# Performance work log

Hardware: AMD Instinct MI355X
Metric: run time of the kernel (lower is better)

Reference implementation:

```python
import jax, jax.numpy as jnp
import numpy as np

B, T, I, H, F = 1024, 15, 256, 512, 8  # batch, seq(=BatchNorm1d(15)), input, hidden, out_features
G = 4 * H  # gate width, PyTorch gate order i,f,g,o


def setup_inputs() -> dict:
    key = jax.random.key(0)
    ks = jax.random.split(key, 10)
    s = lambda k, shape, sc=0.05: (jax.random.normal(k, shape, jnp.float32) * sc)
    return {
        "X": jax.random.normal(ks[0], (B, T, I), jnp.float32),
        # per-head stacked LSTM params (layer 0 and layer 1); bias = b_ih + b_hh combined
        "Wih0": s(ks[1], (F, G, I)), "Whh0": s(ks[2], (F, G, H)), "b0": s(ks[3], (F, G)),
        "Wih1": s(ks[4], (F, G, H)), "Whh1": s(ks[5], (F, G, H)), "b1": s(ks[6], (F, G)),
        # shared affine head: Linear(H,H) -> BatchNorm1d(15) -> ReLU -> Linear(H,1)
        "A1": s(ks[7], (H, H)), "c1": jnp.zeros((H,), jnp.float32),
        "gamma": jnp.ones((T,), jnp.float32), "beta": jnp.zeros((T,), jnp.float32),
        "A2": s(ks[8], (1, H)), "c2": jnp.zeros((1,), jnp.float32),
    }


def _lstm_layer(x, Wih, Whh, b):
    # x: [B,T,Din] -> [B,T,H]; PyTorch LSTM cell, gates ordered i,f,g,o
    xg = jnp.einsum('bti,gi->btg', x, Wih) + b  # precompute input projections [B,T,4H]
    Hh = Whh.shape[1]

    def step(carry, xg_t):
        h, c = carry
        g = xg_t + h @ Whh.T
        i_, f_, g_, o_ = jnp.split(g, 4, axis=-1)
        c = jax.nn.sigmoid(f_) * c + jax.nn.sigmoid(i_) * jnp.tanh(g_)
        h = jax.nn.sigmoid(o_) * jnp.tanh(c)
        return (h, c), h

    h0 = jnp.zeros((x.shape[0], Hh), x.dtype)
    _, hs = jax.lax.scan(step, (h0, h0), jnp.swapaxes(xg, 0, 1))
    return jnp.swapaxes(hs, 0, 1)  # [B,T,H]


def reference(X, Wih0, Whh0, b0, Wih1, Whh1, b1, A1, c1, gamma, beta, A2, c2):
    # F independent 2-layer LSTM stacks, vmapped over the head dim
    def per_head(wih0, whh0, bb0, wih1, whh1, bb1):
        y = _lstm_layer(X, wih0, whh0, bb0)
        return _lstm_layer(y, wih1, whh1, bb1)

    Y = jax.vmap(per_head)(Wih0, Whh0, b0, Wih1, Whh1, b1)  # [F,B,T,H]

    # shared affine head applied per head output (BN stats per head, training mode)
    h1 = jnp.einsum('fbth,oh->fbto', Y, A1) + c1            # [F,B,T,H]
    mean = h1.mean(axis=(1, 3), keepdims=True)              # per (head, channel=T)
    var = h1.var(axis=(1, 3), keepdims=True)                # biased var (torch BN train)
    hn = (h1 - mean) * jax.lax.rsqrt(var + 1e-5)
    hn = hn * gamma[None, None, :, None] + beta[None, None, :, None]
    out = jnp.einsum('fbth,oh->fbto', jax.nn.relu(hn), A2) + c2  # [F,B,T,1]
    return jnp.squeeze(out, -1).transpose(1, 2, 0)          # [B,T,F]
```

## Files before the change

### kernel.cpp

```cpp
#include <hip/hip_runtime.h>
#include <hip/hip_bf16.h>
#include <math.h>

#define Bb 1024
#define Tt 15
#define Ii 256
#define Hh 512
#define Ff 8
#define Gg 2048

typedef __attribute__((ext_vector_type(8))) short short8v;
typedef __attribute__((ext_vector_type(4))) float f32x4;

typedef const __attribute__((address_space(1))) void* gas_ptr;
typedef __attribute__((address_space(3))) void* las_ptr;

__device__ __forceinline__ float sigmoidf_(float x) {
    return __builtin_amdgcn_rcpf(1.0f + __expf(-x));
}
__device__ __forceinline__ float tanhf_(float x) {
    x = fminf(fmaxf(x, -15.0f), 15.0f);
    const float e = __expf(2.0f * x);
    return (e - 1.0f) * __builtin_amdgcn_rcpf(e + 1.0f);
}
__device__ __forceinline__ float bf2f(unsigned short u) {
    return __uint_as_float(((unsigned int)u) << 16);
}
__device__ __forceinline__ unsigned short f2bf(float f) {
    unsigned int u = __float_as_uint(f);
    u += 0x7fffu + ((u >> 16) & 1u);
    return (unsigned short)(u >> 16);
}

__global__ __launch_bounds__(256) void cvt_kernel(const float* __restrict__ in,
                                                  unsigned short* __restrict__ out, int n8) {
    const int i = blockIdx.x * 256 + threadIdx.x;
    if (i < n8) {
        const float4 v0 = ((const float4*)in)[i * 2];
        const float4 v1 = ((const float4*)in)[i * 2 + 1];
        union { unsigned short u[8]; short8v v; } ob;
        ob.u[0] = f2bf(v0.x); ob.u[1] = f2bf(v0.y); ob.u[2] = f2bf(v0.z); ob.u[3] = f2bf(v0.w);
        ob.u[4] = f2bf(v1.x); ob.u[5] = f2bf(v1.y); ob.u[6] = f2bf(v1.z); ob.u[7] = f2bf(v1.w);
        *(short8v*)&out[(size_t)i * 8] = ob.v;
    }
}

__global__ __launch_bounds__(256) void cvt_wperm_kernel(const float* __restrict__ in,
                                                        unsigned short* __restrict__ out,
                                                        int Kc, int nchunks) {
    const int i = blockIdx.x * 256 + threadIdx.x;
    if (i < nchunks) {
        const int k8 = i % Kc;
        const int r  = (i / Kc) & 127;
        const int hb = (i / (Kc * 128)) & 15;
        const int f  = i / (Kc * 128 * 16);
        const int gate = (r >> 4) & 3;
        const int hl = (r & 15) + ((r >> 6) << 4);
        const size_t src = ((size_t)f * Gg + gate * Hh + hb * 32 + hl) * (size_t)(Kc * 8) + k8 * 8;
        const float4 v0 = *(const float4*)(in + src);
        const float4 v1 = *(const float4*)(in + src + 4);
        union { unsigned short u[8]; short8v v; } ob;
        ob.u[0] = f2bf(v0.x); ob.u[1] = f2bf(v0.y); ob.u[2] = f2bf(v0.z); ob.u[3] = f2bf(v0.w);
        ob.u[4] = f2bf(v1.x); ob.u[5] = f2bf(v1.y); ob.u[6] = f2bf(v1.z); ob.u[7] = f2bf(v1.w);
        *(short8v*)&out[(size_t)i * 8] = ob.v;
    }
}

template<int MODE>
__device__ __forceinline__ void step_body(
    bool first, int f, int h0, int b0, int t, int hb, int bb,
    const short* ax, long axs, const short* ah, long ahs,
    const short* __restrict__ wxp, const short* __restrict__ whp,
    const float* __restrict__ bias, unsigned short* __restrict__ cbuf,
    unsigned short* __restrict__ ydst,
    float* __restrict__ part, char* smem)
{
    constexpr int KX = (MODE == 0) ? Ii : Hh;
    constexpr int NX = KX / 64;
    const int NT = (MODE == 2) ? NX : (first ? NX : NX + Hh / 64);

    const int tid = threadIdx.x;
    const int wave = tid >> 6, lane = tid & 63;
    const int wm = (wave >> 1) * 64, wn = (wave & 1) * 64;

    short* sStage = (short*)smem;
    float* pr = (float*)(smem + 65536);

    f32x4 acc[4][4];
#pragma unroll
    for (int i = 0; i < 4; ++i)
#pragma unroll
        for (int j = 0; j < 4; ++j) acc[i][j] = (f32x4){0.f, 0.f, 0.f, 0.f};

    const int srow8 = lane >> 3;
    const int csrc  = (lane & 7) ^ srow8;
    const int frow  = lane & 15, fks = lane >> 4;

    auto stage = [&](int it, int buf) {
        const short* abase; long as; const short* wbase; int K; int kb;
        if (it < NX) { abase = ax; as = axs; wbase = wxp; K = KX; kb = it * 64; }
        else         { abase = ah; as = ahs; wbase = whp; K = Hh; kb = (it - NX) * 64; }
        short* dA = sStage + buf * 16384;
        short* dB = dA + 8192;
#pragma unroll
        for (int i = 0; i < 4; ++i) {
            const int inst = wave * 4 + i;
            const int row = inst * 8 + srow8;
            const short* srcA = abase + (size_t)row * as + kb + csrc * 8;
            __builtin_amdgcn_global_load_lds((gas_ptr)(const void*)srcA,
                (las_ptr)(void*)(dA + inst * 512), 16, 0, 0);
            const short* srcB = wbase + (size_t)row * K + kb + csrc * 8;
            __builtin_amdgcn_global_load_lds((gas_ptr)(const void*)srcB,
                (las_ptr)(void*)(dB + inst * 512), 16, 0, 0);
        }
    };

    auto compute = [&](int buf) {
        const short* bA = sStage + buf * 16384;
        const short* bB = bA + 8192;
        __builtin_amdgcn_s_setprio(1);
#pragma unroll
        for (int ks = 0; ks < 2; ++ks) {
            short8v av[4], bv[4];
#pragma unroll
            for (int i = 0; i < 4; ++i) {
                const int r = wm + i * 16 + frow;
                av[i] = *(const short8v*)&bA[r * 64 + (((fks + ks * 4) ^ (r & 7)) * 8)];
            }
#pragma unroll
            for (int j = 0; j < 4; ++j) {
                const int r = wn + j * 16 + frow;
                bv[j] = *(const short8v*)&bB[r * 64 + (((fks + ks * 4) ^ (r & 7)) * 8)];
            }
#pragma unroll
            for (int i = 0; i < 4; ++i)
#pragma unroll
                for (int j = 0; j < 4; ++j)
                    acc[i][j] = __builtin_amdgcn_mfma_f32_16x16x32_bf16(av[i], bv[j], acc[i][j], 0, 0, 0);
        }
        __builtin_amdgcn_s_setprio(0);
    };

    const int hoff = ((wn >> 6) << 4) + (lane & 15);
    float bi[4] = {0.f, 0.f, 0.f, 0.f};
    if constexpr (MODE != 2) {
#pragma unroll
        for (int g = 0; g < 4; ++g) bi[g] = bias[(size_t)f * Gg + g * Hh + h0 + hoff];
    } else {
#pragma unroll
        for (int j = 0; j < 4; ++j) bi[j] = bias[h0 + wn + j * 16 + (lane & 15)];
    }
    asm volatile("" : "+v"(bi[0]), "+v"(bi[1]), "+v"(bi[2]), "+v"(bi[3]));

    stage(0, 0);
    for (int it = 0; it < NT; ++it) {
        if (it + 1 < NT) {
            stage(it + 1, (it + 1) & 1);
            asm volatile("s_waitcnt vmcnt(8)" ::: "memory");
        } else {
            asm volatile("s_waitcnt vmcnt(0)" ::: "memory");
        }
        __builtin_amdgcn_s_barrier();
        __builtin_amdgcn_sched_barrier(0);
        compute(it & 1);
        __builtin_amdgcn_sched_barrier(0);
        __builtin_amdgcn_s_barrier();
    }

    if constexpr (MODE != 2) {
#pragma unroll
        for (int i = 0; i < 4; ++i)
#pragma unroll
            for (int r = 0; r < 4; ++r) {
                const int b = b0 + wm + i * 16 + ((lane >> 4) << 2) + r;
                const float gi = acc[i][0][r] + bi[0];
                const float gf = acc[i][1][r] + bi[1];
                const float gg = acc[i][2][r] + bi[2];
                const float go = acc[i][3][r] + bi[3];
                const size_t cidx = ((size_t)f * Bb + b) * Hh + h0 + hoff;
                const float cold = first ? 0.f : bf2f(cbuf[cidx]);
                const float cn = sigmoidf_(gf) * cold + sigmoidf_(gi) * tanhf_(gg);
                const float hv = sigmoidf_(go) * tanhf_(cn);
                cbuf[cidx] = f2bf(cn);
                const unsigned short hb2 = f2bf(hv);
                if (MODE == 0)
                    ydst[(((size_t)f * Bb + b) * Tt + t) * Hh + h0 + hoff] = hb2;
                else
                    ydst[cidx] = hb2;
            }
    } else {
        float ssum = 0.f, ssq = 0.f;
#pragma unroll
        for (int i = 0; i < 4; ++i)
#pragma unroll
            for (int r = 0; r < 4; ++r) {
                const int b = b0 + wm + i * 16 + ((lane >> 4) << 2) + r;
                unsigned short* dst = ydst + (((size_t)f * Bb + b) * Tt + t) * Hh;
#pragma unroll
                for (int j = 0; j < 4; ++j) {
                    const int o = h0 + wn + j * 16 + (lane & 15);
                    const unsigned short hb2 = f2bf(acc[i][j][r] + bi[j]);
                    const float hv = bf2f(hb2);
                    ssum += hv; ssq += hv * hv;
                    dst[o] = hb2;
                }
            }
#pragma unroll
        for (int off2 = 32; off2 > 0; off2 >>= 1) {
            ssum += __shfl_down(ssum, off2);
            ssq  += __shfl_down(ssq,  off2);
        }
        if (lane == 0) { pr[wave * 2] = ssum; pr[wave * 2 + 1] = ssq; }
        __syncthreads();
        if (tid == 0) {
            float S = 0.f, Q = 0.f;
#pragma unroll
            for (int w = 0; w < 4; ++w) { S += pr[w * 2]; Q += pr[w * 2 + 1]; }
            const size_t pi = (((size_t)f * Tt + t) * 4 + hb) * 8 + bb;
            part[pi * 2] = S; part[pi * 2 + 1] = Q;
        }
    }
}

__global__ __launch_bounds__(256) void step_merged(
    const short* __restrict__ Xbf, short* __restrict__ ybuf,
    short* __restrict__ h1A, short* __restrict__ h1B,
    const short* __restrict__ W0x, const short* __restrict__ W0h,
    const short* __restrict__ W1x, const short* __restrict__ W1h,
    const short* __restrict__ A1bf,
    const float* __restrict__ b0p, const float* __restrict__ b1p,
    const float* __restrict__ c1v,
    unsigned short* __restrict__ c0buf, unsigned short* __restrict__ c1buf,
    float* __restrict__ part, int d)
{
    __shared__ __align__(16) char smem[65600];
    const int f = blockIdx.x;
    const int zz = blockIdx.z;

    if (zz < 8) {
        const int t = d;
        if (t >= Tt) return;
        const int hb = blockIdx.y, h0 = hb * 32, b0 = zz * 128;
        const bool first = (t == 0);
        const short* ax = Xbf + ((size_t)b0 * Tt + t) * Ii;
        const short* ah = first ? nullptr
                                : ybuf + (((size_t)f * Bb + b0) * Tt + (t - 1)) * Hh;
        step_body<0>(first, f, h0, b0, t, hb, zz,
                     ax, (long)Tt * Ii, ah, (long)Tt * Hh,
                     W0x + ((size_t)f * 16 + hb) * 128 * Ii,
                     W0h + ((size_t)f * 16 + hb) * 128 * Hh,
                     b0p, c0buf, (unsigned short*)ybuf, part, smem);
    } else if (zz < 16) {
        const int t = d - 1;
        if (t < 0 || t >= Tt) return;
        const int bb = zz - 8;
        const int hb = blockIdx.y, h0 = hb * 32, b0 = bb * 128;
        const bool first = (t == 0);
        short* hn = (t & 1) ? h1A : h1B;
        const short* hp = (t & 1) ? h1B : h1A;
        const short* ax = ybuf + (((size_t)f * Bb + b0) * Tt + t) * Hh;
        const short* ah = first ? nullptr : hp + ((size_t)f * Bb + b0) * Hh;
        step_body<1>(first, f, h0, b0, t, hb, bb,
                     ax, (long)Tt * Hh, ah, (long)Hh,
                     W1x + ((size_t)f * 16 + hb) * 128 * Hh,
                     W1h + ((size_t)f * 16 + hb) * 128 * Hh,
                     b1p, c1buf, (unsigned short*)hn, part, smem);
    } else {
        const int t = d - 2;
        if (t < 0) return;
        const int hb = blockIdx.y & 3, h0 = hb * 128;
        const int bb = (zz - 16) * 4 + (blockIdx.y >> 2), b0 = bb * 128;
        const short* hn = (t & 1) ? h1A : h1B;
        const short* ax = hn + ((size_t)f * Bb + b0) * Hh;
        step_body<2>(false, f, h0, b0, t, hb, bb,
                     ax, (long)Hh, nullptr, 0L,
                     A1bf + (size_t)h0 * Hh, nullptr,
                     c1v, nullptr, (unsigned short*)ybuf, part, smem);
    }
}

__global__ void stats_combine_kernel(const float* __restrict__ part, float* __restrict__ stats)
{
    const int i = threadIdx.x;
    if (i < Ff * Tt) {
        float s = 0.f, q = 0.f;
        for (int j = 0; j < 32; ++j) { s += part[(i * 32 + j) * 2]; q += part[(i * 32 + j) * 2 + 1]; }
        const float n = (float)((size_t)Bb * Hh);
        const float mean = s / n;
        const float var  = q / n - mean * mean;
        stats[i * 2]     = mean;
        stats[i * 2 + 1] = rsqrtf(var + 1e-5f);
    }
}

__global__ __launch_bounds__(256) void out_kernel(
    const unsigned short* __restrict__ htmp, const float* __restrict__ stats,
    const float* __restrict__ gamma, const float* __restrict__ beta,
    const float* __restrict__ A2, const float* __restrict__ c2,
    float* __restrict__ out)
{
    const int wave = threadIdx.x >> 6;
    const int lane = threadIdx.x & 63;
    const size_t row = (size_t)blockIdx.x * 4 + wave;
    const int t = (int)(row % Tt);
    const size_t fb = row / Tt;
    const int b = (int)(fb % Bb);
    const int f = (int)(fb / Bb);

    const float mean = stats[(f * Tt + t) * 2];
    const float inv  = stats[(f * Tt + t) * 2 + 1];
    const float ga = gamma[t], be = beta[t];
    const unsigned short* hrow = htmp + row * Hh;

    union { float4 f4; unsigned short u[8]; } hv;
    hv.f4 = *(const float4*)(hrow + lane * 8);
    const float4 a0 = *(const float4*)(A2 + lane * 8);
    const float4 a1 = *(const float4*)(A2 + lane * 8 + 4);
    const float a2v[8] = {a0.x, a0.y, a0.z, a0.w, a1.x, a1.y, a1.z, a1.w};

    float acc = 0.f;
#pragma unroll
    for (int j = 0; j < 8; ++j) {
        const float x = (bf2f(hv.u[j]) - mean) * inv * ga + be;
        acc += fmaxf(x, 0.f) * a2v[j];
    }
#pragma unroll
    for (int off = 32; off > 0; off >>= 1) acc += __shfl_down(acc, off);
    if (lane == 0) out[(size_t)b * Tt * Ff + (size_t)t * Ff + f] = acc + c2[0];
}

extern "C" void kernel_launch(void* const* d_in, const int* in_sizes, int n_in,
                              void* d_out, int out_size, void* d_ws, size_t ws_size,
                              hipStream_t stream) {
    const float* X     = (const float*)d_in[0];
    const float* Wih0  = (const float*)d_in[1];
    const float* Whh0  = (const float*)d_in[2];
    const float* b0p   = (const float*)d_in[3];
    const float* Wih1  = (const float*)d_in[4];
    const float* Whh1  = (const float*)d_in[5];
    const float* b1p   = (const float*)d_in[6];
    const float* A1    = (const float*)d_in[7];
    const float* c1v   = (const float*)d_in[8];
    const float* gamma = (const float*)d_in[9];
    const float* beta  = (const float*)d_in[10];
    const float* A2    = (const float*)d_in[11];
    const float* c2    = (const float*)d_in[12];
    float* out = (float*)d_out;

    char* ws = (char*)d_ws;
    size_t off = 0;
    short* Xbf    = (short*)(ws + off); off += (size_t)Bb * Tt * Ii * 2;
    short* Wih0bf = (short*)(ws + off); off += (size_t)Ff * Gg * Ii * 2;
    short* Whh0bf = (short*)(ws + off); off += (size_t)Ff * Gg * Hh * 2;
    short* Wih1bf = (short*)(ws + off); off += (size_t)Ff * Gg * Hh * 2;
    short* Whh1bf = (short*)(ws + off); off += (size_t)Ff * Gg * Hh * 2;
    short* A1bf   = (short*)(ws + off); off += (size_t)Hh * Hh * 2;
    short* ybuf   = (short*)(ws + off); off += (size_t)Ff * Bb * Tt * Hh * 2;
    short* h1A    = (short*)(ws + off); off += (size_t)Ff * Bb * Hh * 2;
    short* h1B    = (short*)(ws + off); off += (size_t)Ff * Bb * Hh * 2;
    unsigned short* c0buf = (unsigned short*)(ws + off); off += (size_t)Ff * Bb * Hh * 2;
    unsigned short* c1buf = (unsigned short*)(ws + off); off += (size_t)Ff * Bb * Hh * 2;
    float* part   = (float*)(ws + off); off += (size_t)Ff * Tt * 32 * 2 * 4;
    float* stats  = (float*)(ws + off); off += (size_t)Ff * Tt * 2 * 4;

    const dim3 blk(256);
    cvt_kernel<<<dim3((Bb * Tt * Ii / 8 + 255) / 256), blk, 0, stream>>>(X, (unsigned short*)Xbf, Bb * Tt * Ii / 8);
    cvt_wperm_kernel<<<dim3((Ff * Gg * Ii / 8 + 255) / 256), blk, 0, stream>>>(
        Wih0, (unsigned short*)Wih0bf, Ii / 8, Ff * Gg * Ii / 8);
    cvt_wperm_kernel<<<dim3((Ff * Gg * Hh / 8 + 255) / 256), blk, 0, stream>>>(
        Whh0, (unsigned short*)Whh0bf, Hh / 8, Ff * Gg * Hh / 8);
    cvt_wperm_kernel<<<dim3((Ff * Gg * Hh / 8 + 255) / 256), blk, 0, stream>>>(
        Wih1, (unsigned short*)Wih1bf, Hh / 8, Ff * Gg * Hh / 8);
    cvt_wperm_kernel<<<dim3((Ff * Gg * Hh / 8 + 255) / 256), blk, 0, stream>>>(
        Whh1, (unsigned short*)Whh1bf, Hh / 8, Ff * Gg * Hh / 8);
    cvt_kernel<<<dim3((Hh * Hh / 8 + 255) / 256), blk, 0, stream>>>(A1, (unsigned short*)A1bf, Hh * Hh / 8);

    const dim3 gmerged(Ff, 16, 18);
    for (int d = 0; d <= Tt + 1; ++d) {
        step_merged<<<gmerged, blk, 0, stream>>>(
            Xbf, ybuf, h1A, h1B,
            Wih0bf, Whh0bf, Wih1bf, Whh1bf, A1bf,
            b0p, b1p, c1v, c0buf, c1buf, part, d);
    }

    stats_combine_kernel<<<dim3(1), dim3(128), 0, stream>>>(part, stats);
    out_kernel<<<dim3(Ff * Bb * Tt / 4), blk, 0, stream>>>((const unsigned short*)ybuf, stats,
        gamma, beta, A2, c2, out);
    (void)in_sizes; (void)n_in; (void)out_size; (void)ws_size;
}
```

Baseline: 1.372 ms.

## Load A operand directly into registers, halve LDS staging, raise occupancy

The activation (A) tile is no longer staged through LDS. Each wave now loads its A fragments straight from global memory into registers every iteration, and only the weight (B) tile is still double-buffered in LDS. This halves shared memory per block and adds a launch bound of 3 blocks per CU, aiming for higher occupancy and fewer LDS round-trips. The trade-off is that the A loads are not prefetched, so their latency is exposed inside each iteration. Waves that share rows also fetch the same A data twice from global memory, and the register cap may cause spills.

```diff
diff --git a/kernel.cpp b/kernel.cpp
--- a/kernel.cpp
+++ b/kernel.cpp
@@ -84,7 +84,7 @@
     const int wm = (wave >> 1) * 64, wn = (wave & 1) * 64;
 
     short* sStage = (short*)smem;
-    float* pr = (float*)(smem + 65536);
+    float* pr = (float*)(smem + 32768);
 
     f32x4 acc[4][4];
 #pragma unroll
@@ -96,37 +96,40 @@
     const int csrc  = (lane & 7) ^ srow8;
     const int frow  = lane & 15, fks = lane >> 4;
 
-    auto stage = [&](int it, int buf) {
-        const short* abase; long as; const short* wbase; int K; int kb;
-        if (it < NX) { abase = ax; as = axs; wbase = wxp; K = KX; kb = it * 64; }
-        else         { abase = ah; as = ahs; wbase = whp; K = Hh; kb = (it - NX) * 64; }
-        short* dA = sStage + buf * 16384;
-        short* dB = dA + 8192;
+    auto stageB = [&](int it, int buf) {
+        const short* wbase; int K; int kb;
+        if (it < NX) { wbase = wxp; K = KX; kb = it * 64; }
+        else         { wbase = whp; K = Hh; kb = (it - NX) * 64; }
+        short* dB = sStage + buf * 8192;
 #pragma unroll
         for (int i = 0; i < 4; ++i) {
             const int inst = wave * 4 + i;
             const int row = inst * 8 + srow8;
-            const short* srcA = abase + (size_t)row * as + kb + csrc * 8;
-            __builtin_amdgcn_global_load_lds((gas_ptr)(const void*)srcA,
-                (las_ptr)(void*)(dA + inst * 512), 16, 0, 0);
             const short* srcB = wbase + (size_t)row * K + kb + csrc * 8;
             __builtin_amdgcn_global_load_lds((gas_ptr)(const void*)srcB,
                 (las_ptr)(void*)(dB + inst * 512), 16, 0, 0);
         }
     };
 
+    short8v avr[2][4];
+    auto loadA = [&](int it) {
+        const short* abase; long as; int kb;
+        if (it < NX) { abase = ax; as = axs; kb = it * 64; }
+        else         { abase = ah; as = ahs; kb = (it - NX) * 64; }
+#pragma unroll
+        for (int ks = 0; ks < 2; ++ks)
+#pragma unroll
+            for (int i = 0; i < 4; ++i)
+                avr[ks][i] = *(const short8v*)(abase
+                    + (size_t)(wm + i * 16 + frow) * as + kb + (fks + ks * 4) * 8);
+    };
+
     auto compute = [&](int buf) {
-        const short* bA = sStage + buf * 16384;
-        const short* bB = bA + 8192;
+        const short* bB = sStage + buf * 8192;
         __builtin_amdgcn_s_setprio(1);
 #pragma unroll
         for (int ks = 0; ks < 2; ++ks) {
-            short8v av[4], bv[4];
-#pragma unroll
-            for (int i = 0; i < 4; ++i) {
-                const int r = wm + i * 16 + frow;
-                av[i] = *(const short8v*)&bA[r * 64 + (((fks + ks * 4) ^ (r & 7)) * 8)];
-            }
+            short8v bv[4];
 #pragma unroll
             for (int j = 0; j < 4; ++j) {
                 const int r = wn + j * 16 + frow;
@@ -136,7 +139,7 @@
             for (int i = 0; i < 4; ++i)
 #pragma unroll
                 for (int j = 0; j < 4; ++j)
-                    acc[i][j] = __builtin_amdgcn_mfma_f32_16x16x32_bf16(av[i], bv[j], acc[i][j], 0, 0, 0);
+                    acc[i][j] = __builtin_amdgcn_mfma_f32_16x16x32_bf16(avr[ks][i], bv[j], acc[i][j], 0, 0, 0);
         }
         __builtin_amdgcn_s_setprio(0);
     };
@@ -152,11 +155,12 @@
     }
     asm volatile("" : "+v"(bi[0]), "+v"(bi[1]), "+v"(bi[2]), "+v"(bi[3]));
 
-    stage(0, 0);
+    stageB(0, 0);
     for (int it = 0; it < NT; ++it) {
+        loadA(it);
         if (it + 1 < NT) {
-            stage(it + 1, (it + 1) & 1);
-            asm volatile("s_waitcnt vmcnt(8)" ::: "memory");
+            stageB(it + 1, (it + 1) & 1);
+            asm volatile("s_waitcnt vmcnt(4)" ::: "memory");
         } else {
             asm volatile("s_waitcnt vmcnt(0)" ::: "memory");
         }
@@ -222,7 +226,7 @@
     }
 }
 
-__global__ __launch_bounds__(256) void step_merged(
+__global__ __launch_bounds__(256, 3) void step_merged(
     const short* __restrict__ Xbf, short* __restrict__ ybuf,
     short* __restrict__ h1A, short* __restrict__ h1B,
     const short* __restrict__ W0x, const short* __restrict__ W0h,
@@ -233,7 +237,7 @@
     unsigned short* __restrict__ c0buf, unsigned short* __restrict__ c1buf,
     float* __restrict__ part, int d)
 {
-    __shared__ __align__(16) char smem[65600];
+    __shared__ __align__(16) char smem[32768 + 64];
     const int f = blockIdx.x;
     const int zz = blockIdx.z;
 
```

New measurement: 2.140 ms. +56.0%, slower.

## Single-buffer weight tiles to shrink LDS and fit three blocks per CU

Applied to the files above, without the earlier changes.

The weight (B) staging tile is now single-buffered, while the activation (A) tile stays double-buffered. This cuts LDS use from about 64KB to 48KB per block. Launch bounds now request three blocks per CU, to raise occupancy and hide latency across blocks. In exchange, the next weight tile is only loaded after the current compute and barrier, so its global-load latency is no longer overlapped within a block. The tighter register budget could also cause spills.

```diff
diff --git a/kernel.cpp b/kernel.cpp
--- a/kernel.cpp
+++ b/kernel.cpp
@@ -84,7 +84,7 @@
     const int wm = (wave >> 1) * 64, wn = (wave & 1) * 64;
 
     short* sStage = (short*)smem;
-    float* pr = (float*)(smem + 65536);
+    float* pr = (float*)(smem + 49152);
 
     f32x4 acc[4][4];
 #pragma unroll
@@ -96,12 +96,11 @@
     const int csrc  = (lane & 7) ^ srow8;
     const int frow  = lane & 15, fks = lane >> 4;
 
-    auto stage = [&](int it, int buf) {
-        const short* abase; long as; const short* wbase; int K; int kb;
-        if (it < NX) { abase = ax; as = axs; wbase = wxp; K = KX; kb = it * 64; }
-        else         { abase = ah; as = ahs; wbase = whp; K = Hh; kb = (it - NX) * 64; }
-        short* dA = sStage + buf * 16384;
-        short* dB = dA + 8192;
+    auto stageA = [&](int it, int buf) {
+        const short* abase; long as; int kb;
+        if (it < NX) { abase = ax; as = axs; kb = it * 64; }
+        else         { abase = ah; as = ahs; kb = (it - NX) * 64; }
+        short* dA = sStage + buf * 8192;
 #pragma unroll
         for (int i = 0; i < 4; ++i) {
             const int inst = wave * 4 + i;
@@ -109,15 +108,27 @@
             const short* srcA = abase + (size_t)row * as + kb + csrc * 8;
             __builtin_amdgcn_global_load_lds((gas_ptr)(const void*)srcA,
                 (las_ptr)(void*)(dA + inst * 512), 16, 0, 0);
+        }
+    };
+
+    auto stageB = [&](int it) {
+        const short* wbase; int K; int kb;
+        if (it < NX) { wbase = wxp; K = KX; kb = it * 64; }
+        else         { wbase = whp; K = Hh; kb = (it - NX) * 64; }
+        short* dB = sStage + 16384;
+#pragma unroll
+        for (int i = 0; i < 4; ++i) {
+            const int inst = wave * 4 + i;
+            const int row = inst * 8 + srow8;
             const short* srcB = wbase + (size_t)row * K + kb + csrc * 8;
             __builtin_amdgcn_global_load_lds((gas_ptr)(const void*)srcB,
                 (las_ptr)(void*)(dB + inst * 512), 16, 0, 0);
         }
     };
 
-    auto compute = [&](int buf) {
-        const short* bA = sStage + buf * 16384;
-        const short* bB = bA + 8192;
+    auto compute = [&](int abuf) {
+        const short* bA = sStage + abuf * 8192;
+        const short* bB = sStage + 16384;
         __builtin_amdgcn_s_setprio(1);
 #pragma unroll
         for (int ks = 0; ks < 2; ++ks) {
@@ -152,11 +163,12 @@
     }
     asm volatile("" : "+v"(bi[0]), "+v"(bi[1]), "+v"(bi[2]), "+v"(bi[3]));
 
-    stage(0, 0);
+    stageA(0, 0);
+    stageB(0);
     for (int it = 0; it < NT; ++it) {
         if (it + 1 < NT) {
-            stage(it + 1, (it + 1) & 1);
-            asm volatile("s_waitcnt vmcnt(8)" ::: "memory");
+            stageA(it + 1, (it + 1) & 1);
+            asm volatile("s_waitcnt vmcnt(4)" ::: "memory");
         } else {
             asm volatile("s_waitcnt vmcnt(0)" ::: "memory");
         }
@@ -165,6 +177,7 @@
         compute(it & 1);
         __builtin_amdgcn_sched_barrier(0);
         __builtin_amdgcn_s_barrier();
+        if (it + 1 < NT) stageB(it + 1);
     }
 
     if constexpr (MODE != 2) {
@@ -222,7 +235,7 @@
     }
 }
 
-__global__ __launch_bounds__(256) void step_merged(
+__global__ __launch_bounds__(256, 3) void step_merged(
     const short* __restrict__ Xbf, short* __restrict__ ybuf,
     short* __restrict__ h1A, short* __restrict__ h1B,
     const short* __restrict__ W0x, const short* __restrict__ W0h,
@@ -233,7 +246,7 @@
     unsigned short* __restrict__ c0buf, unsigned short* __restrict__ c1buf,
     float* __restrict__ part, int d)
 {
-    __shared__ __align__(16) char smem[65600];
+    __shared__ __align__(16) char smem[49152 + 64];
     const int f = blockIdx.x;
     const int zz = blockIdx.z;
 
```

After: 1.246 ms. 1.1x faster.
